# Performance work log

Hardware: AMD Instinct MI355X
Metric: run time of the kernel (lower is better)

## Reference

```python
import jax, jax.numpy as jnp
import numpy as np

PADDING = 300
NMS_THRESH = 0.5


def bbox_transform_inv(boxes, deltas):
    # boxes: (N,4) x1,y1,x2,y2 ; deltas: (N,4*C) -> (N,4*C) decoded boxes
    w = boxes[:, 2] - boxes[:, 0] + 1.0
    h = boxes[:, 3] - boxes[:, 1] + 1.0
    cx = boxes[:, 0] + 0.5 * w
    cy = boxes[:, 1] + 0.5 * h
    dx, dy = deltas[:, 0::4], deltas[:, 1::4]
    dw, dh = deltas[:, 2::4], deltas[:, 3::4]
    pcx = dx * w[:, None] + cx[:, None]
    pcy = dy * h[:, None] + cy[:, None]
    pw = jnp.exp(dw) * w[:, None]
    ph = jnp.exp(dh) * h[:, None]
    out = jnp.stack([pcx - 0.5 * pw, pcy - 0.5 * ph,
                     pcx + 0.5 * pw, pcy + 0.5 * ph], axis=2)  # (N,C,4)
    return out.reshape(boxes.shape[0], -1)


def clip_boxes(boxes, hw):
    # hw = (H, W); boxes (N, 4*C)
    b = boxes.reshape(boxes.shape[0], -1, 4)
    x1 = jnp.clip(b[..., 0], 0.0, hw[1] - 1.0)
    y1 = jnp.clip(b[..., 1], 0.0, hw[0] - 1.0)
    x2 = jnp.clip(b[..., 2], 0.0, hw[1] - 1.0)
    y2 = jnp.clip(b[..., 3], 0.0, hw[0] - 1.0)
    return jnp.stack([x1, y1, x2, y2], axis=2).reshape(boxes.shape[0], -1)


def nms(boxes, scores, max_out, thresh):
    # Greedy NMS: sequential argmax + IoU suppression (fixed max_out iters).
    N = boxes.shape[0]
    x1, y1, x2, y2 = boxes[:, 0], boxes[:, 1], boxes[:, 2], boxes[:, 3]
    areas = (x2 - x1 + 1.0) * (y2 - y1 + 1.0)
    neg_inf = jnp.array(-jnp.inf, boxes.dtype)

    def step(s, _):
        i = jnp.argmax(s)
        valid = s[i] > neg_inf
        xx1 = jnp.maximum(x1[i], x1)
        yy1 = jnp.maximum(y1[i], y1)
        xx2 = jnp.minimum(x2[i], x2)
        yy2 = jnp.minimum(y2[i], y2)
        inter = jnp.maximum(xx2 - xx1 + 1.0, 0.0) * jnp.maximum(yy2 - yy1 + 1.0, 0.0)
        iou = inter / (areas[i] + areas - inter)
        suppress = (iou > thresh) | (jnp.arange(N) == i)
        s = jnp.where(suppress, neg_inf, s)
        return s, (i, valid)

    _, (idx, valid) = jax.lax.scan(step, scores, None, length=max_out)
    return idx, valid


def reference(metadata, deltas, proposals, scores, masks):
    N = proposals.shape[1]
    C = scores.shape[2]
    prop = proposals.reshape(-1, 4)
    boxes = prop / metadata[0, 2]                       # undo image scale
    d = deltas.reshape(N, -1)
    pred = bbox_transform_inv(boxes, d)                 # (N, 4C)
    pred = clip_boxes(pred, metadata[0, :2])
    sc = scores.reshape(N, C)
    top = jnp.argmax(sc, axis=1)                        # most probable class
    predc = pred.reshape(N, C, 4)
    pbox = jnp.take_along_axis(predc, top[:, None, None], axis=1)[:, 0, :]  # (N,4)
    max_scores = jnp.max(sc[:, 1:], axis=1)             # skip background col
    idx, valid = nms(jax.lax.stop_gradient(pbox),
                     jax.lax.stop_gradient(max_scores), PADDING, NMS_THRESH)
    vf = valid.astype(pbox.dtype)
    out_boxes = pbox[idx] * vf[:, None]                 # (300,4), zero padded
    out_scores = sc[idx] * vf[:, None]                  # (300,C)
    out_masks = masks[0][idx] * vf[:, None, None, None] # (300,mh,mw,mc)
    return out_boxes[None], out_scores[None], out_masks[None]


def setup_inputs() -> dict:
    key = jax.random.key(0)
    k1, k2, k3, k4, k5 = jax.random.split(key, 5)
    N, C, MH, MW, MC = 6000, 81, 14, 14, 81
    H, W, SCALE = 600.0, 800.0, 1.6
    metadata = jnp.array([[H, W, SCALE]], dtype=jnp.float32)
    # proposals: valid boxes inside the scaled image
    xy = jax.random.uniform(k1, (N, 2), jnp.float32) * jnp.array([W - 120.0, H - 120.0], jnp.float32)
    wh = jax.random.uniform(k2, (N, 2), jnp.float32) * 100.0 + 16.0
    proposals = jnp.concatenate([xy, xy + wh], axis=1)[None] * SCALE  # (1,N,4)
    deltas = jax.random.normal(k3, (1, N, 4 * C), jnp.float32) * 0.1
    scores = jax.random.uniform(k4, (1, N, C), jnp.float32)
    masks = jax.random.uniform(k5, (1, N, MH, MW, MC), jnp.float32)
    return {"metadata": metadata, "deltas": deltas, "proposals": proposals,
            "scores": scores, "masks": masks}
```

## Files before the change

kernel.cpp:

```cpp
#include <hip/hip_runtime.h>
#include <math.h>

#pragma STDC FP_CONTRACT OFF

#define N 6000
#define NPAD 6144
#define C 81
#define PADDING 300
#define NMS_THRESH 0.5f
#define MASK_ELEMS (14 * 14 * 81)
#define MASK_W 96
#define NCHUNK 8
#define CHUNK 750
#define LOOK 8

typedef unsigned long long u64;

__global__ void decode_kernel(const float* __restrict__ meta,
                              const float* __restrict__ deltas,
                              const float* __restrict__ proposals,
                              const float* __restrict__ scores,
                              float* __restrict__ pbox,
                              float* __restrict__ area,
                              u64* __restrict__ skey) {
    int n = blockIdx.x * blockDim.x + threadIdx.x;
    if (n >= N) return;

    float Hm = meta[0], Wm = meta[1], scale = meta[2];

    float b0 = proposals[n * 4 + 0] / scale;
    float b1 = proposals[n * 4 + 1] / scale;
    float b2 = proposals[n * 4 + 2] / scale;
    float b3 = proposals[n * 4 + 3] / scale;
    float w = b2 - b0 + 1.0f;
    float h = b3 - b1 + 1.0f;
    float cx = b0 + 0.5f * w;
    float cy = b1 + 0.5f * h;

    const float* sr = scores + n * C;
    int top = 0;
    float best = sr[0];
    float ms = -INFINITY;
    for (int c = 1; c < C; ++c) {
        float s = sr[c];
        if (s > best) { best = s; top = c; }
        ms = fmaxf(ms, s);
    }

    const float* dr = deltas + n * (4 * C) + 4 * top;
    float dx = dr[0], dy = dr[1], dw = dr[2], dh = dr[3];
    float pcx = dx * w + cx;
    float pcy = dy * h + cy;
    float pw = expf(dw) * w;
    float ph = expf(dh) * h;
    float x1 = pcx - 0.5f * pw;
    float y1 = pcy - 0.5f * ph;
    float x2 = pcx + 0.5f * pw;
    float y2 = pcy + 0.5f * ph;
    x1 = fminf(fmaxf(x1, 0.0f), Wm - 1.0f);
    y1 = fminf(fmaxf(y1, 0.0f), Hm - 1.0f);
    x2 = fminf(fmaxf(x2, 0.0f), Wm - 1.0f);
    y2 = fminf(fmaxf(y2, 0.0f), Hm - 1.0f);

    pbox[n * 4 + 0] = x1;
    pbox[n * 4 + 1] = y1;
    pbox[n * 4 + 2] = x2;
    pbox[n * 4 + 3] = y2;
    area[n] = (x2 - x1 + 1.0f) * (y2 - y1 + 1.0f);

    unsigned int b = __float_as_uint(ms);
    unsigned int u = b ^ ((b & 0x80000000u) ? 0xFFFFFFFFu : 0x80000000u);
    skey[n] = ((u64)u << 32) | (unsigned int)(~n);
}

__global__ void rank_kernel(const u64* __restrict__ skey,
                            int* __restrict__ rank_part) {
    __shared__ u64 lk[CHUNK];
    int chunk = blockIdx.y;
    int t = threadIdx.x;
    int j0 = chunk * CHUNK;
    for (int j = t; j < CHUNK; j += 256) lk[j] = skey[j0 + j];
    __syncthreads();

    int i = blockIdx.x * 256 + t;
    if (i >= N) return;
    u64 mykey = skey[i];
    int cnt = 0;
    for (int j = 0; j < CHUNK; ++j) cnt += (lk[j] > mykey) ? 1 : 0;
    rank_part[chunk * NPAD + i] = cnt;
}

__global__ void scatter_kernel(const int* __restrict__ rank_part,
                               const float* __restrict__ pbox,
                               const float* __restrict__ area,
                               int* __restrict__ sidx,
                               float* __restrict__ sx1, float* __restrict__ sy1,
                               float* __restrict__ sx2, float* __restrict__ sy2,
                               float* __restrict__ sarea) {
    int i = blockIdx.x * blockDim.x + threadIdx.x;
    if (i >= N) return;
    int r = 0;
    for (int c = 0; c < NCHUNK; ++c) r += rank_part[c * NPAD + i];
    sidx[r] = i;
    sx1[r] = pbox[i * 4 + 0];
    sy1[r] = pbox[i * 4 + 1];
    sx2[r] = pbox[i * 4 + 2];
    sy2[r] = pbox[i * 4 + 3];
    sarea[r] = area[i];
}

__global__ void __launch_bounds__(256) iou_kernel(const float* __restrict__ sx1,
                                                  const float* __restrict__ sy1,
                                                  const float* __restrict__ sx2,
                                                  const float* __restrict__ sy2,
                                                  const float* __restrict__ sarea,
                                                  u64* __restrict__ mask) {
    int p = blockIdx.x * 4 + (threadIdx.x >> 6);
    int lane = threadIdx.x & 63;
    if (p >= N) return;

    float wx1 = sx1[p], wy1 = sy1[p], wx2 = sx2[p], wy2 = sy2[p];
    float war = sarea[p];
    u64* row = mask + (size_t)p * MASK_W;

    for (int w = 0; w < 94; ++w) {
        int q = w * 64 + lane;
        float xx1 = fmaxf(wx1, sx1[q]);
        float yy1 = fmaxf(wy1, sy1[q]);
        float xx2 = fminf(wx2, sx2[q]);
        float yy2 = fminf(wy2, sy2[q]);
        float inter = fmaxf(xx2 - xx1 + 1.0f, 0.0f) * fmaxf(yy2 - yy1 + 1.0f, 0.0f);
        float iou = inter / (war + sarea[q] - inter);
        u64 bal = __ballot(iou > NMS_THRESH);
        if (lane == 0) row[w] = bal;
    }
}

__global__ void scan_kernel(const u64* __restrict__ mask,
                            const int* __restrict__ sidx,
                            int* __restrict__ out_idx,
                            float* __restrict__ out_valid) {
    int lane = threadIdx.x;
    int w0 = 2 * lane, w1 = 2 * lane + 1;

    u64 m_lo = (w0 < 93) ? 0ULL : (w0 == 93 ? 0xFFFF000000000000ULL : ~0ULL);
    u64 m_hi = (w1 < 93) ? 0ULL : (w1 == 93 ? 0xFFFF000000000000ULL : ~0ULL);

    u64 cx[LOOK], cy[LOOK];
#pragma unroll
    for (int k = 0; k < LOOK; ++k) { cx[k] = 0; cy[k] = 0; }
    int base = -1000000;

    int r = 0;
    while (r < PADDING) {
        u64 z0 = ~m_lo, z1 = ~m_hi;
        u64 bal = __ballot((z0 | z1) != 0ULL);
        if (bal == 0ULL) break;
        int lsrc = (int)__ffsll(bal) - 1;
        int local = (z0 != 0ULL) ? ((int)__ffsll(z0) - 1) : (64 + (int)__ffsll(z1) - 1);
        int p = __shfl(lane * 128 + local, lsrc);

        if (p > base + (LOOK - 1)) {
            base = p;
            if (lane < 48) {
#pragma unroll
                for (int k = 0; k < LOOK; ++k) {
                    int rowp = min(p + k, N - 1);
                    const u64* rp = mask + (size_t)rowp * MASK_W + 2 * lane;
                    cx[k] = rp[0];
                    cy[k] = rp[1];
                }
            }
        }
        int s = p - base;
        u64 vx = cx[0], vy = cy[0];
#pragma unroll
        for (int k = 1; k < LOOK; ++k) {
            if (s == k) { vx = cx[k]; vy = cy[k]; }
        }
        if (lane < 48) { m_lo |= vx; m_hi |= vy; }
        if (lane == 0) { out_idx[r] = sidx[p]; out_valid[r] = 1.0f; }
        ++r;
    }
    for (; r < PADDING; ++r) {
        if (lane == 0) { out_idx[r] = 0; out_valid[r] = 0.0f; }
    }
}

__global__ void gather_kernel(const float* __restrict__ pbox,
                              const float* __restrict__ scores,
                              const float* __restrict__ masks,
                              const int* __restrict__ idx,
                              const float* __restrict__ valid,
                              float* __restrict__ out) {
    int b = blockIdx.x;
    int tid = threadIdx.x;
    int i = idx[b];
    float vf = valid[b];

    if (tid < 4) out[b * 4 + tid] = pbox[i * 4 + tid] * vf;
    if (tid < C) out[PADDING * 4 + b * C + tid] = scores[i * C + tid] * vf;

    const float4* src = (const float4*)(masks + (size_t)i * MASK_ELEMS);
    float4* dst = (float4*)(out + PADDING * 4 + PADDING * C + (size_t)b * MASK_ELEMS);
    for (int m = tid; m < MASK_ELEMS / 4; m += 256) {
        float4 v = src[m];
        dst[m] = make_float4(v.x * vf, v.y * vf, v.z * vf, v.w * vf);
    }
}

extern "C" void kernel_launch(void* const* d_in, const int* in_sizes, int n_in,
                              void* d_out, int out_size, void* d_ws, size_t ws_size,
                              hipStream_t stream) {
    const float* meta      = (const float*)d_in[0];
    const float* deltas    = (const float*)d_in[1];
    const float* proposals = (const float*)d_in[2];
    const float* scores    = (const float*)d_in[3];
    const float* masks     = (const float*)d_in[4];
    float* out = (float*)d_out;

    char* ws = (char*)d_ws;
    u64*   mask      = (u64*)(ws);
    u64*   skey      = (u64*)(ws + 4608000);
    float* pbox      = (float*)(ws + 4657152);
    float* area      = (float*)(ws + 4753152);
    int*   rank_part = (int*)(ws + 4777152);
    int*   sidx      = (int*)(ws + 4973760);
    float* sx1       = (float*)(ws + 4998336);
    float* sy1       = (float*)(ws + 5022912);
    float* sx2       = (float*)(ws + 5047488);
    float* sy2       = (float*)(ws + 5072064);
    float* sarea     = (float*)(ws + 5096640);
    int*   out_idx   = (int*)(ws + 5121216);
    float* out_valid = (float*)(ws + 5122416);

    decode_kernel<<<24, 256, 0, stream>>>(meta, deltas, proposals, scores, pbox, area, skey);
    rank_kernel<<<dim3(24, NCHUNK), 256, 0, stream>>>(skey, rank_part);
    scatter_kernel<<<24, 256, 0, stream>>>(rank_part, pbox, area, sidx, sx1, sy1, sx2, sy2, sarea);
    iou_kernel<<<1500, 256, 0, stream>>>(sx1, sy1, sx2, sy2, sarea, mask);
    scan_kernel<<<1, 64, 0, stream>>>(mask, sidx, out_idx, out_valid);
    gather_kernel<<<PADDING, 256, 0, stream>>>(pbox, scores, masks, out_idx, out_valid, out);
}
```

Measured before the change: 614.6 us.

## Parallelize decode per wavefront, skip lower IoU words, double-buffer scan row prefetch

Decode now assigns one 64-lane wavefront per proposal and finds the top class and max score with a shuffle reduction, replacing the serial per-thread loop over 81 scores. The IoU kernel computes only mask words at or after the row's own word, halving the work. The serial scan keeps two 8-row buffers and slides them, so a reload is needed less often on its critical path. The sorted-index lookup moves from the scan into the gather kernel.

```diff
diff --git a/kernel.cpp b/kernel.cpp
--- a/kernel.cpp
+++ b/kernel.cpp
@@ -12,7 +12,6 @@
 #define MASK_W 96
 #define NCHUNK 8
 #define CHUNK 750
-#define LOOK 8
 
 typedef unsigned long long u64;
 
@@ -23,54 +22,67 @@
                               float* __restrict__ pbox,
                               float* __restrict__ area,
                               u64* __restrict__ skey) {
-    int n = blockIdx.x * blockDim.x + threadIdx.x;
+    int n = blockIdx.x * 4 + (threadIdx.x >> 6);
+    int lane = threadIdx.x & 63;
     if (n >= N) return;
 
-    float Hm = meta[0], Wm = meta[1], scale = meta[2];
-
-    float b0 = proposals[n * 4 + 0] / scale;
-    float b1 = proposals[n * 4 + 1] / scale;
-    float b2 = proposals[n * 4 + 2] / scale;
-    float b3 = proposals[n * 4 + 3] / scale;
-    float w = b2 - b0 + 1.0f;
-    float h = b3 - b1 + 1.0f;
-    float cx = b0 + 0.5f * w;
-    float cy = b1 + 0.5f * h;
-
     const float* sr = scores + n * C;
-    int top = 0;
-    float best = sr[0];
-    float ms = -INFINITY;
-    for (int c = 1; c < C; ++c) {
-        float s = sr[c];
-        if (s > best) { best = s; top = c; }
-        ms = fmaxf(ms, s);
-    }
-
-    const float* dr = deltas + n * (4 * C) + 4 * top;
-    float dx = dr[0], dy = dr[1], dw = dr[2], dh = dr[3];
-    float pcx = dx * w + cx;
-    float pcy = dy * h + cy;
-    float pw = expf(dw) * w;
-    float ph = expf(dh) * h;
-    float x1 = pcx - 0.5f * pw;
-    float y1 = pcy - 0.5f * ph;
-    float x2 = pcx + 0.5f * pw;
-    float y2 = pcy + 0.5f * ph;
-    x1 = fminf(fmaxf(x1, 0.0f), Wm - 1.0f);
-    y1 = fminf(fmaxf(y1, 0.0f), Hm - 1.0f);
-    x2 = fminf(fmaxf(x2, 0.0f), Wm - 1.0f);
-    y2 = fminf(fmaxf(y2, 0.0f), Hm - 1.0f);
-
-    pbox[n * 4 + 0] = x1;
-    pbox[n * 4 + 1] = y1;
-    pbox[n * 4 + 2] = x2;
-    pbox[n * 4 + 3] = y2;
-    area[n] = (x2 - x1 + 1.0f) * (y2 - y1 + 1.0f);
-
-    unsigned int b = __float_as_uint(ms);
-    unsigned int u = b ^ ((b & 0x80000000u) ? 0xFFFFFFFFu : 0x80000000u);
-    skey[n] = ((u64)u << 32) | (unsigned int)(~n);
+    float s0 = sr[lane];
+    float s1 = (lane < C - 64) ? sr[lane + 64] : -INFINITY;
+
+    float av = s0;
+    int ai = lane;
+    if (s1 > av) { av = s1; ai = lane + 64; }
+    float mv = (lane >= 1) ? s0 : -INFINITY;
+    mv = fmaxf(mv, s1);
+
+    for (int off = 32; off >= 1; off >>= 1) {
+        float ov = __shfl_down(av, off);
+        int oi = __shfl_down(ai, off);
+        float om = __shfl_down(mv, off);
+        if (ov > av || (ov == av && oi < ai)) { av = ov; ai = oi; }
+        mv = fmaxf(mv, om);
+    }
+
+    if (lane == 0) {
+        int top = ai;
+        float ms = mv;
+
+        float Hm = meta[0], Wm = meta[1], scale = meta[2];
+        float b0 = proposals[n * 4 + 0] / scale;
+        float b1 = proposals[n * 4 + 1] / scale;
+        float b2 = proposals[n * 4 + 2] / scale;
+        float b3 = proposals[n * 4 + 3] / scale;
+        float w = b2 - b0 + 1.0f;
+        float h = b3 - b1 + 1.0f;
+        float cx = b0 + 0.5f * w;
+        float cy = b1 + 0.5f * h;
+
+        const float* dr = deltas + n * (4 * C) + 4 * top;
+        float dx = dr[0], dy = dr[1], dw = dr[2], dh = dr[3];
+        float pcx = dx * w + cx;
+        float pcy = dy * h + cy;
+        float pw = expf(dw) * w;
+        float ph = expf(dh) * h;
+        float x1 = pcx - 0.5f * pw;
+        float y1 = pcy - 0.5f * ph;
+        float x2 = pcx + 0.5f * pw;
+        float y2 = pcy + 0.5f * ph;
+        x1 = fminf(fmaxf(x1, 0.0f), Wm - 1.0f);
+        y1 = fminf(fmaxf(y1, 0.0f), Hm - 1.0f);
+        x2 = fminf(fmaxf(x2, 0.0f), Wm - 1.0f);
+        y2 = fminf(fmaxf(y2, 0.0f), Hm - 1.0f);
+
+        pbox[n * 4 + 0] = x1;
+        pbox[n * 4 + 1] = y1;
+        pbox[n * 4 + 2] = x2;
+        pbox[n * 4 + 3] = y2;
+        area[n] = (x2 - x1 + 1.0f) * (y2 - y1 + 1.0f);
+
+        unsigned int b = __float_as_uint(ms);
+        unsigned int u = b ^ ((b & 0x80000000u) ? 0xFFFFFFFFu : 0x80000000u);
+        skey[n] = ((u64)u << 32) | (unsigned int)(~n);
+    }
 }
 
 __global__ void rank_kernel(const u64* __restrict__ skey,
@@ -123,7 +135,7 @@
     float war = sarea[p];
     u64* row = mask + (size_t)p * MASK_W;
 
-    for (int w = 0; w < 94; ++w) {
+    for (int w = (p >> 6); w < 94; ++w) {
         int q = w * 64 + lane;
         float xx1 = fmaxf(wx1, sx1[q]);
         float yy1 = fmaxf(wy1, sy1[q]);
@@ -136,9 +148,23 @@
     }
 }
 
+__device__ __forceinline__ void load_rows8(const u64* __restrict__ mask,
+                                           int rowbase, int lane,
+                                           u64* bx, u64* by) {
+    if (lane < 48) {
+#pragma unroll
+        for (int k = 0; k < 8; ++k) {
+            int r = rowbase + k;
+            r = (r < N) ? r : (N - 1);
+            const u64* q = mask + (size_t)r * MASK_W + 2 * lane;
+            bx[k] = q[0];
+            by[k] = q[1];
+        }
+    }
+}
+
 __global__ void scan_kernel(const u64* __restrict__ mask,
-                            const int* __restrict__ sidx,
-                            int* __restrict__ out_idx,
+                            int* __restrict__ out_pos,
                             float* __restrict__ out_valid) {
     int lane = threadIdx.x;
     int w0 = 2 * lane, w1 = 2 * lane + 1;
@@ -146,10 +172,13 @@
     u64 m_lo = (w0 < 93) ? 0ULL : (w0 == 93 ? 0xFFFF000000000000ULL : ~0ULL);
     u64 m_hi = (w1 < 93) ? 0ULL : (w1 == 93 ? 0xFFFF000000000000ULL : ~0ULL);
 
-    u64 cx[LOOK], cy[LOOK];
-#pragma unroll
-    for (int k = 0; k < LOOK; ++k) { cx[k] = 0; cy[k] = 0; }
-    int base = -1000000;
+    u64 ax[8], ay[8], bx[8], by[8];
+#pragma unroll
+    for (int k = 0; k < 8; ++k) { ax[k] = 0; ay[k] = 0; bx[k] = 0; by[k] = 0; }
+
+    int base = 0;
+    load_rows8(mask, 0, lane, ax, ay);
+    load_rows8(mask, 8, lane, bx, by);
 
     int r = 0;
     while (r < PADDING) {
@@ -158,44 +187,43 @@
         if (bal == 0ULL) break;
         int lsrc = (int)__ffsll(bal) - 1;
         int local = (z0 != 0ULL) ? ((int)__ffsll(z0) - 1) : (64 + (int)__ffsll(z1) - 1);
-        int p = __shfl(lane * 128 + local, lsrc);
-
-        if (p > base + (LOOK - 1)) {
+        int p = __builtin_amdgcn_readlane(lane * 128 + local, lsrc);
+
+        if (p >= base + 16) {
             base = p;
-            if (lane < 48) {
-#pragma unroll
-                for (int k = 0; k < LOOK; ++k) {
-                    int rowp = min(p + k, N - 1);
-                    const u64* rp = mask + (size_t)rowp * MASK_W + 2 * lane;
-                    cx[k] = rp[0];
-                    cy[k] = rp[1];
-                }
-            }
+            load_rows8(mask, base, lane, ax, ay);
+            load_rows8(mask, base + 8, lane, bx, by);
+        } else if (p >= base + 8) {
+            base += 8;
+#pragma unroll
+            for (int k = 0; k < 8; ++k) { ax[k] = bx[k]; ay[k] = by[k]; }
+            load_rows8(mask, base + 8, lane, bx, by);
         }
         int s = p - base;
-        u64 vx = cx[0], vy = cy[0];
-#pragma unroll
-        for (int k = 1; k < LOOK; ++k) {
-            if (s == k) { vx = cx[k]; vy = cy[k]; }
+        u64 vx = ax[0], vy = ay[0];
+#pragma unroll
+        for (int k = 1; k < 8; ++k) {
+            if (s == k) { vx = ax[k]; vy = ay[k]; }
         }
         if (lane < 48) { m_lo |= vx; m_hi |= vy; }
-        if (lane == 0) { out_idx[r] = sidx[p]; out_valid[r] = 1.0f; }
+        if (lane == 0) { out_pos[r] = p; out_valid[r] = 1.0f; }
         ++r;
     }
     for (; r < PADDING; ++r) {
-        if (lane == 0) { out_idx[r] = 0; out_valid[r] = 0.0f; }
+        if (lane == 0) { out_pos[r] = 0; out_valid[r] = 0.0f; }
     }
 }
 
 __global__ void gather_kernel(const float* __restrict__ pbox,
                               const float* __restrict__ scores,
                               const float* __restrict__ masks,
-                              const int* __restrict__ idx,
+                              const int* __restrict__ sidx,
+                              const int* __restrict__ out_pos,
                               const float* __restrict__ valid,
                               float* __restrict__ out) {
     int b = blockIdx.x;
     int tid = threadIdx.x;
-    int i = idx[b];
+    int i = sidx[out_pos[b]];
     float vf = valid[b];
 
     if (tid < 4) out[b * 4 + tid] = pbox[i * 4 + tid] * vf;
@@ -231,13 +259,13 @@
     float* sx2       = (float*)(ws + 5047488);
     float* sy2       = (float*)(ws + 5072064);
     float* sarea     = (float*)(ws + 5096640);
-    int*   out_idx   = (int*)(ws + 5121216);
+    int*   out_pos   = (int*)(ws + 5121216);
     float* out_valid = (float*)(ws + 5122416);
 
-    decode_kernel<<<24, 256, 0, stream>>>(meta, deltas, proposals, scores, pbox, area, skey);
+    decode_kernel<<<1500, 256, 0, stream>>>(meta, deltas, proposals, scores, pbox, area, skey);
     rank_kernel<<<dim3(24, NCHUNK), 256, 0, stream>>>(skey, rank_part);
     scatter_kernel<<<24, 256, 0, stream>>>(rank_part, pbox, area, sidx, sx1, sy1, sx2, sy2, sarea);
     iou_kernel<<<1500, 256, 0, stream>>>(sx1, sy1, sx2, sy2, sarea, mask);
-    scan_kernel<<<1, 64, 0, stream>>>(mask, sidx, out_idx, out_valid);
-    gather_kernel<<<PADDING, 256, 0, stream>>>(pbox, scores, masks, out_idx, out_valid, out);
-}
+    scan_kernel<<<1, 64, 0, stream>>>(mask, out_pos, out_valid);
+    gather_kernel<<<PADDING, 256, 0, stream>>>(pbox, scores, masks, sidx, out_pos, out_valid, out);
+}
```

Measured after the change: 602.5 us. 1.02x faster.
